# Kernel tuning notes

Hardware: AMD Instinct MI355X
Metric: run time of the kernel (lower is better)

## Reference

```python
import jax, jax.numpy as jnp
import numpy as np
from jax import lax

C = 768
SHIFT_DISTANCES = (1, 2, 3)


def _layernorm(x, g, b, eps=1e-5):
    m = jnp.mean(x, axis=-1, keepdims=True)
    v = jnp.mean((x - m) ** 2, axis=-1, keepdims=True)
    return (x - m) * lax.rsqrt(v + eps) * g + b


def setup_inputs() -> dict:
    key = jax.random.key(0)
    ks = jax.random.split(key, 16)
    B, T, N = 8, 16, 197
    inp = {
        "x": jax.random.normal(ks[0], (B * T, N, C), dtype=jnp.float32),
        "ln_g": jnp.ones((C,), jnp.float32),
        "ln_b": jnp.zeros((C,), jnp.float32),
        "gate_w": jax.random.normal(ks[1], (C, C), jnp.float32) * 0.02,
        "gate_b": jnp.zeros((C,), jnp.float32),
        "proj_w1": jax.random.normal(ks[2], (C, C), jnp.float32) * 0.02,
        "proj_b1": jnp.zeros((C,), jnp.float32),
        "proj_w2": jax.random.normal(ks[3], (C, C), jnp.float32) * 0.02,
        "proj_b2": jnp.zeros((C,), jnp.float32),
        "fusion_w": jnp.ones((len(SHIFT_DISTANCES),), jnp.float32),
        "num_frames": T,
    }
    for i, d in enumerate(SHIFT_DISTANCES):
        k = 2 * d + 1
        # depthwise Conv1d weight: (out=C, in/groups=1, k)
        inp[f"conv_w{i}"] = jax.random.normal(ks[4 + i], (C, 1, k), jnp.float32) * (1.0 / np.sqrt(k))
        inp[f"conv_b{i}"] = jnp.zeros((C,), jnp.float32)
    return inp


def _branch(x4, conv_w, conv_b, d, ln_g, ln_b, gate_w, gate_b):
    # x4: [B, T, N, C]
    B, T, N, Cc = x4.shape
    p = Cc // 3  # past / future split; static gets the remainder
    x_norm = jax.nn.relu(_layernorm(x4, ln_g, ln_b))
    # [B, T, N, C] -> [B*N, C, T] for depthwise conv over time
    x_1d = x_norm.transpose(0, 2, 3, 1).reshape(B * N, Cc, T)
    feat = lax.conv_general_dilated(
        x_1d, conv_w, window_strides=(1,), padding=[(d, d)],
        dimension_numbers=("NCH", "OIH", "NCH"), feature_group_count=Cc,
    ) + conv_b[None, :, None]
    feat = feat.reshape(B, N, Cc, T).transpose(0, 3, 1, 2)  # [B, T, N, C]
    gate = jax.nn.sigmoid(jnp.einsum("btnc,cd->btnd", feat, gate_w) + gate_b)
    y = gate * x4  # channelwise split-and-multiply fuses into one op
    y_past, y_future, y_static = y[..., :p], y[..., p:2 * p], y[..., 2 * p:]
    s = min(d, T)
    out_past = jnp.pad(y_past[:, s:], ((0, 0), (0, s), (0, 0), (0, 0)))  # lshift
    out_future = jnp.pad(y_future[:, :T - s], ((0, 0), (s, 0), (0, 0), (0, 0)))  # rshift
    return jnp.concatenate([out_past, out_future, y_static], axis=-1)


def reference(x, ln_g, ln_b, gate_w, gate_b, proj_w1, proj_b1, proj_w2, proj_b2,
              fusion_w, conv_w0, conv_b0, conv_w1, conv_b1, conv_w2, conv_b2,
              num_frames):
    B_T, N, Cc = x.shape
    T = num_frames
    B = B_T // T
    x4 = x.reshape(B, T, N, Cc)
    convs = [(conv_w0, conv_b0), (conv_w1, conv_b1), (conv_w2, conv_b2)]
    outs = jnp.stack([
        _branch(x4, cw, cb, d, ln_g, ln_b, gate_w, gate_b)
        for (cw, cb), d in zip(convs, SHIFT_DISTANCES)
    ], axis=0)  # [3, B, T, N, C]
    w = jax.nn.softmax(fusion_w)[:, None, None, None, None]
    fused = jnp.sum(w * outs, axis=0).reshape(B_T, N, Cc)
    h = jnp.einsum("bnc,cd->bnd", fused, proj_w1) + proj_b1
    h = jax.nn.gelu(h, approximate=False)
    h = jnp.einsum("bnc,cd->bnd", h, proj_w2) + proj_b2
    return x + h
```

## Files before the change

### kernel.cpp

```cpp
#include <hip/hip_runtime.h>
#include <math.h>


#define MROWS 25216
#define CD    768
#define NTOK  197
#define TFR   16

typedef __attribute__((ext_vector_type(8))) short short8;
typedef __attribute__((ext_vector_type(4))) float floatx4;
typedef unsigned int u32;

__device__ __forceinline__ unsigned short f2bf(float f) {
    union { float f; unsigned u; } v; v.f = f;
    unsigned r = v.u + 0x7FFFu + ((v.u >> 16) & 1u);
    return (unsigned short)(r >> 16);
}
__device__ __forceinline__ float bf2f(unsigned short h) {
    union { unsigned u; float f; } v; v.u = ((unsigned)h) << 16;
    return v.f;
}

__device__ __forceinline__ void gl2lds16(const void* g, void* l) {
    __builtin_amdgcn_global_load_lds(
        (__attribute__((address_space(1))) void*)(unsigned long long)g,
        (__attribute__((address_space(3))) void*)(u32)(unsigned long long)l,
        16, 0, 0);
}

__global__ __launch_bounds__(256)
void ln_relu_kernel(const float* __restrict__ x, const float* __restrict__ g,
                    const float* __restrict__ b, unsigned short* __restrict__ xn,
                    unsigned short* __restrict__ xb) {
    int row = blockIdx.x;
    int tid = threadIdx.x;
    const float* xr = x + (size_t)row * CD;
    float v0 = xr[tid], v1 = xr[tid + 256], v2 = xr[tid + 512];
    float s = v0 + v1 + v2;
    __shared__ float red[8];
#pragma unroll
    for (int off = 32; off; off >>= 1) s += __shfl_down(s, off, 64);
    int lane = tid & 63, w = tid >> 6;
    if (lane == 0) red[w] = s;
    __syncthreads();
    float mean = (red[0] + red[1] + red[2] + red[3]) * (1.0f / CD);
    float d0 = v0 - mean, d1 = v1 - mean, d2 = v2 - mean;
    float s2 = d0 * d0 + d1 * d1 + d2 * d2;
#pragma unroll
    for (int off = 32; off; off >>= 1) s2 += __shfl_down(s2, off, 64);
    if (lane == 0) red[4 + w] = s2;
    __syncthreads();
    float var = (red[4] + red[5] + red[6] + red[7]) * (1.0f / CD);
    float inv = rsqrtf(var + 1e-5f);
    unsigned short* xo = xn + (size_t)row * CD;
    unsigned short* xc = xb + (size_t)row * CD;
    float o0 = fmaxf(d0 * inv * g[tid]       + b[tid],       0.0f);
    float o1 = fmaxf(d1 * inv * g[tid + 256] + b[tid + 256], 0.0f);
    float o2 = fmaxf(d2 * inv * g[tid + 512] + b[tid + 512], 0.0f);
    xo[tid] = f2bf(o0); xo[tid + 256] = f2bf(o1); xo[tid + 512] = f2bf(o2);
    xc[tid] = f2bf(v0); xc[tid + 256] = f2bf(v1); xc[tid + 512] = f2bf(v2);
}

template <int D>
__device__ __forceinline__
void dw_body(const unsigned short* __restrict__ xn, const float* __restrict__ cw,
             const float* __restrict__ cb, unsigned short* __restrict__ feat) {
    constexpr int KK = 2 * D + 1;
    int gid = blockIdx.x * 256 + threadIdx.x;
    int bn = gid / 96;
    int cg = gid - bn * 96;
    int c0 = cg * 8;
    int b = bn / NTOK;
    size_t base = ((size_t)b * TFR * NTOK + (bn - b * NTOK)) * CD + c0;
    const size_t tstride = (size_t)NTOK * CD;

    short8 u[TFR];
#pragma unroll
    for (int t = 0; t < TFR; ++t)
        u[t] = *(const short8*)(xn + base + (size_t)t * tstride);

    float wgt[8][KK], bb[8];
#pragma unroll
    for (int q = 0; q < 8; ++q) {
        bb[q] = cb[c0 + q];
#pragma unroll
        for (int j = 0; j < KK; ++j) wgt[q][j] = cw[(c0 + q) * KK + j];
    }

#pragma unroll
    for (int t = 0; t < TFR; ++t) {
        float acc[8];
#pragma unroll
        for (int q = 0; q < 8; ++q) acc[q] = bb[q];
#pragma unroll
        for (int j = 0; j < KK; ++j) {
            int tj = t + j - D;
            if (tj < 0 || tj >= TFR) continue;
#pragma unroll
            for (int q = 0; q < 8; ++q)
                acc[q] += bf2f((unsigned short)u[tj][q]) * wgt[q][j];
        }
        short8 o;
#pragma unroll
        for (int q = 0; q < 8; ++q) o[q] = (short)f2bf(acc[q]);
        *(short8*)(feat + base + (size_t)t * tstride) = o;
    }
}

__global__ __launch_bounds__(256)
void dwconv_all(const unsigned short* __restrict__ xn,
                const float* __restrict__ cw0, const float* __restrict__ cb0,
                const float* __restrict__ cw1, const float* __restrict__ cb1,
                const float* __restrict__ cw2, const float* __restrict__ cb2,
                unsigned short* __restrict__ f1, unsigned short* __restrict__ f2,
                unsigned short* __restrict__ f3) {
    if (blockIdx.y == 0)      dw_body<1>(xn, cw0, cb0, f1);
    else if (blockIdx.y == 1) dw_body<2>(xn, cw1, cb1, f2);
    else                      dw_body<3>(xn, cw2, cb2, f3);
}

__global__ __launch_bounds__(256)
void wprep3_kernel(const float* __restrict__ w0, const float* __restrict__ w1,
                   const float* __restrict__ w2, unsigned short* __restrict__ t0,
                   unsigned short* __restrict__ t1, unsigned short* __restrict__ t2) {
    const float* w = blockIdx.y == 0 ? w0 : blockIdx.y == 1 ? w1 : w2;
    unsigned short* wt = blockIdx.y == 0 ? t0 : blockIdx.y == 1 ? t1 : t2;
    int gid = blockIdx.x * 256 + threadIdx.x;
    int n = gid / CD, k = gid - n * CD;
    wt[gid] = f2bf(w[(size_t)k * CD + n]);
}

__global__ __launch_bounds__(256)
void fuse_kernel(const unsigned short* __restrict__ y1,
                 const unsigned short* __restrict__ y2,
                 const unsigned short* __restrict__ y3,
                 unsigned short* __restrict__ fused) {
    int gid = blockIdx.x * 256 + threadIdx.x;
    int m = gid / 96;
    int kk = (gid - m * 96) * 8;
    int t = (m / NTOK) & 15;
    float vals[8] = {0.f, 0.f, 0.f, 0.f, 0.f, 0.f, 0.f, 0.f};
    const unsigned short* ys[3] = {y1, y2, y3};
#pragma unroll
    for (int d = 1; d <= 3; ++d) {
        int src; bool ok;
        if (kk < 256)      { src = m + d * NTOK; ok = (t + d) < TFR; }
        else if (kk < 512) { src = m - d * NTOK; ok = (t - d) >= 0; }
        else               { src = m;            ok = true; }
        if (ok) {
            short8 u = *(const short8*)(ys[d - 1] + (size_t)src * CD + kk);
#pragma unroll
            for (int e = 0; e < 8; ++e) vals[e] += bf2f((unsigned short)u[e]);
        }
    }
    short8 o;
#pragma unroll
    for (int e = 0; e < 8; ++e) o[e] = (short)f2bf(vals[e]);
    *(short8*)(fused + (size_t)m * CD + kk) = o;
}

template <int EPI>
__global__ __launch_bounds__(256)
void gemm_kernel(const unsigned short* __restrict__ A,
                 const unsigned short* __restrict__ Bt,
                 const float* __restrict__ bias,
                 const unsigned short* __restrict__ xb,
                 const float* __restrict__ xf,
                 float* __restrict__ outf,
                 unsigned short* __restrict__ outh0,
                 unsigned short* __restrict__ outh1,
                 unsigned short* __restrict__ outh2,
                 const float* __restrict__ fw) {
    __shared__ __align__(16) char smem[65536];
    unsigned short (*As)[128 * 32] = (unsigned short (*)[128 * 32])smem;
    unsigned short (*Bs)[128 * 32] = (unsigned short (*)[128 * 32])(smem + 32768);
    float (*fE)[132] = (float (*)[132])smem;

    int tid  = threadIdx.x;
    int m0   = blockIdx.x * 128;
    int n0   = blockIdx.y * 128;
    int widx = blockIdx.x / (MROWS / 128);
    int wave = tid >> 6, lane = tid & 63;
    int wm   = (wave >> 1) * 64, wn = (wave & 1) * 64;
    int quad = lane >> 4, l16 = lane & 15;
    int r4   = lane >> 2;
    int ckx  = (((lane & 3) ^ ((lane >> 3) & 3)) * 8);
    int rdsl = (quad ^ ((l16 >> 1) & 3)) * 8;

    const size_t arow = (size_t)(m0 + wave * 16 + r4) * CD + ckx;
    const size_t brow = (size_t)(n0 + wave * 16 + r4) * CD + ckx;
    const size_t skip = (size_t)64 * CD;

    floatx4 acc[4][4];
#pragma unroll
    for (int i = 0; i < 4; ++i)
#pragma unroll
        for (int j = 0; j < 4; ++j) acc[i][j] = (floatx4){0.f, 0.f, 0.f, 0.f};

    auto stage_h = [&](int t, int b, int h) {
        const size_t ko = (size_t)t * 32;
        gl2lds16(A  + arow + h * skip + ko, &As[b][(wave + h * 4) * 512]);
        gl2lds16(Bt + brow + h * skip + ko, &Bs[b][(wave + h * 4) * 512]);
    };
    auto stage = [&](int t, int b) { stage_h(t, b, 0); stage_h(t, b, 1); };

    constexpr int NT = CD / 32;

    auto kstep = [&](int t, bool doStage) {
        int b = t & 3;
        short8 af[4], bfr[4];
#pragma unroll
        for (int i = 0; i < 4; ++i)
            af[i] = *(const short8*)(&As[b][(wm + i * 16 + l16) * 32 + rdsl]);
        bfr[0] = *(const short8*)(&Bs[b][(wn + 0 * 16 + l16) * 32 + rdsl]);
        bfr[1] = *(const short8*)(&Bs[b][(wn + 1 * 16 + l16) * 32 + rdsl]);
        if (doStage) stage_h(t + 3, (t + 3) & 3, 0);
        asm volatile("s_waitcnt lgkmcnt(0)" ::: "memory");
        __builtin_amdgcn_sched_barrier(0);
        __builtin_amdgcn_s_setprio(1);
#pragma unroll
        for (int i = 0; i < 4; ++i) {
            acc[i][0] = __builtin_amdgcn_mfma_f32_16x16x32_bf16(af[i], bfr[0], acc[i][0], 0, 0, 0);
            acc[i][1] = __builtin_amdgcn_mfma_f32_16x16x32_bf16(af[i], bfr[1], acc[i][1], 0, 0, 0);
        }
        __builtin_amdgcn_s_setprio(0);
        __builtin_amdgcn_s_barrier();
        __builtin_amdgcn_sched_barrier(0);
        bfr[2] = *(const short8*)(&Bs[b][(wn + 2 * 16 + l16) * 32 + rdsl]);
        bfr[3] = *(const short8*)(&Bs[b][(wn + 3 * 16 + l16) * 32 + rdsl]);
        if (doStage) stage_h(t + 3, (t + 3) & 3, 1);
        asm volatile("s_waitcnt lgkmcnt(0)" ::: "memory");
        __builtin_amdgcn_sched_barrier(0);
        __builtin_amdgcn_s_setprio(1);
#pragma unroll
        for (int i = 0; i < 4; ++i) {
            acc[i][2] = __builtin_amdgcn_mfma_f32_16x16x32_bf16(af[i], bfr[2], acc[i][2], 0, 0, 0);
            acc[i][3] = __builtin_amdgcn_mfma_f32_16x16x32_bf16(af[i], bfr[3], acc[i][3], 0, 0, 0);
        }
        __builtin_amdgcn_s_setprio(0);
    };

    stage(0, 0);
    stage(1, 1);
    stage(2, 2);
    for (int t = 0; t < NT - 2; ++t) {
        asm volatile("s_waitcnt vmcnt(8)" ::: "memory");
        __builtin_amdgcn_s_barrier();
        __builtin_amdgcn_sched_barrier(0);
        kstep(t, t + 3 < NT);
    }
    asm volatile("s_waitcnt vmcnt(4)" ::: "memory");
    __builtin_amdgcn_s_barrier();
    __builtin_amdgcn_sched_barrier(0);
    kstep(NT - 2, false);
    asm volatile("s_waitcnt vmcnt(0)" ::: "memory");
    __builtin_amdgcn_s_barrier();
    __builtin_amdgcn_sched_barrier(0);
    kstep(NT - 1, false);

    float wd = 0.f;
    unsigned short* outh = outh0;
    if (EPI == 0) {
        float f0 = fw[0], f1 = fw[1], f2 = fw[2];
        float mx = fmaxf(f0, fmaxf(f1, f2));
        float e0 = expf(f0 - mx), e1 = expf(f1 - mx), e2 = expf(f2 - mx);
        float inv = 1.f / (e0 + e1 + e2);
        wd = (widx == 0 ? e0 : widx == 1 ? e1 : e2) * inv;
        outh = widx == 0 ? outh0 : widx == 1 ? outh1 : outh2;
    }
    const size_t lshift = (size_t)widx * MROWS * CD;

#pragma unroll
    for (int p = 0; p < 2; ++p) {
        __syncthreads();
        if (wm == p * 64) {
#pragma unroll
            for (int j = 0; j < 4; ++j) {
                int col = wn + j * 16 + l16;
                float bc = bias[n0 + col];
#pragma unroll
                for (int i = 0; i < 4; ++i)
#pragma unroll
                    for (int r = 0; r < 4; ++r)
                        fE[i * 16 + quad * 4 + r][col] = acc[i][j][r] + bc;
            }
        }
        __syncthreads();
#pragma unroll
        for (int it = 0; it < 4; ++it) {
            int lr   = it * 16 + (tid >> 4);
            int cg   = tid & 15;
            size_t grow = (size_t)(m0 + p * 64 + lr);
            int gcol = n0 + cg * 8;
            size_t idx = grow * CD + gcol - lshift;
            floatx4 v0 = *(const floatx4*)&fE[lr][cg * 8];
            floatx4 v1 = *(const floatx4*)&fE[lr][cg * 8 + 4];
            if (EPI == 0) {
                short8 xv = *(const short8*)(xb + idx);
                short8 o;
#pragma unroll
                for (int e = 0; e < 8; ++e) {
                    float vv = e < 4 ? v0[e] : v1[e - 4];
                    float gte = 1.f / (1.f + expf(-vv));
                    o[e] = (short)f2bf(wd * gte * bf2f((unsigned short)xv[e]));
                }
                *(short8*)(outh + idx) = o;
            } else if (EPI == 1) {
                short8 o;
#pragma unroll
                for (int e = 0; e < 8; ++e) {
                    float vv = e < 4 ? v0[e] : v1[e - 4];
                    float gl = 0.5f * vv * (1.0f + erff(vv * 0.70710678118f));
                    o[e] = (short)f2bf(gl);
                }
                *(short8*)(outh + idx) = o;
            } else {
                floatx4 x0 = *(const floatx4*)(xf + idx);
                floatx4 x1 = *(const floatx4*)(xf + idx + 4);
#pragma unroll
                for (int e = 0; e < 4; ++e) { v0[e] += x0[e]; v1[e] += x1[e]; }
                *(floatx4*)(outf + idx)     = v0;
                *(floatx4*)(outf + idx + 4) = v1;
            }
        }
    }
}

extern "C" void kernel_launch(void* const* d_in, const int* in_sizes, int n_in,
                              void* d_out, int out_size, void* d_ws, size_t ws_size,
                              hipStream_t stream) {
    const float* x      = (const float*)d_in[0];
    const float* ln_g   = (const float*)d_in[1];
    const float* ln_b   = (const float*)d_in[2];
    const float* gate_w = (const float*)d_in[3];
    const float* gate_b = (const float*)d_in[4];
    const float* pw1    = (const float*)d_in[5];
    const float* pb1    = (const float*)d_in[6];
    const float* pw2    = (const float*)d_in[7];
    const float* pb2    = (const float*)d_in[8];
    const float* fw     = (const float*)d_in[9];
    const float* cw[3]  = {(const float*)d_in[11], (const float*)d_in[13], (const float*)d_in[15]};
    const float* cb[3]  = {(const float*)d_in[12], (const float*)d_in[14], (const float*)d_in[16]};

    char* ws = (char*)d_ws;
    const size_t SB = (size_t)MROWS * CD * 2;
    unsigned short* gwt  = (unsigned short*)(ws + 0);
    unsigned short* p1t  = (unsigned short*)(ws + 1179648);
    unsigned short* p2t  = (unsigned short*)(ws + 2359296);
    unsigned short* xn   = (unsigned short*)(ws + 3538944);
    unsigned short* xb   = (unsigned short*)(ws + 3538944 + SB);
    unsigned short* f1   = (unsigned short*)(ws + 3538944 + 2 * SB);
    unsigned short* f2   = (unsigned short*)(ws + 3538944 + 3 * SB);
    unsigned short* f3   = (unsigned short*)(ws + 3538944 + 4 * SB);
    unsigned short* y1    = xn;
    unsigned short* y2    = f1;
    unsigned short* y3    = f2;
    unsigned short* fused = f3;
    unsigned short* h1    = xn;

    dim3 wg(2304, 3);
    wprep3_kernel<<<wg, 256, 0, stream>>>(gate_w, pw1, pw2, gwt, p1t, p2t);
    ln_relu_kernel<<<MROWS, 256, 0, stream>>>(x, ln_g, ln_b, xn, xb);

    dim3 dg(591, 3);
    dwconv_all<<<dg, 256, 0, stream>>>(xn, cw[0], cb[0], cw[1], cb[1], cw[2], cb[2],
                                       f1, f2, f3);

    dim3 gg3(591, 6);
    unsigned short* y2s = (unsigned short*)(ws + 3538944 + 5 * SB);
    unsigned short* y3s = (unsigned short*)(ws + 3538944 + 6 * SB);
    gemm_kernel<0><<<gg3, 256, 0, stream>>>(f1, gwt, gate_b, xb, nullptr,
                                            nullptr, y1, y2s, y3s, fw);

    fuse_kernel<<<9456, 256, 0, stream>>>(y1, y2s, y3s, fused);

    dim3 gg(197, 6);
    gemm_kernel<1><<<gg, 256, 0, stream>>>(fused, p1t, pb1, nullptr, nullptr,
                                           nullptr, h1, nullptr, nullptr, nullptr);
    gemm_kernel<2><<<gg, 256, 0, stream>>>(h1, p2t, pb2, nullptr, x,
                                           (float*)d_out, nullptr, nullptr, nullptr, nullptr);
}
```

Measured before the change: 549.5 us.

## Enlarge GEMM tiles to 128x256 with 8 waves, BK=64 and triple buffering

Rewrites the bf16 MFMA GEMM to use 128x256 output tiles computed by 512 threads (8 waves in a 2x4 layout), a K step of 64 with a new XOR swizzle, and a 3-stage LDS ring in 144 KB of dynamic shared memory. The goal is more reuse of each A tile across output columns and fewer, larger K iterations, which cuts global traffic and barriers per FLOP. The cost is one block per CU because of the large LDS footprint, a grid half as wide along N, and a wider single-pass epilogue staging area.

```diff
diff --git a/kernel.cpp b/kernel.cpp
--- a/kernel.cpp
+++ b/kernel.cpp
@@ -160,7 +160,7 @@
 }
 
 template <int EPI>
-__global__ __launch_bounds__(256)
+__global__ __launch_bounds__(512)
 void gemm_kernel(const unsigned short* __restrict__ A,
                  const unsigned short* __restrict__ Bt,
                  const float* __restrict__ bias,
@@ -171,25 +171,15 @@
                  unsigned short* __restrict__ outh1,
                  unsigned short* __restrict__ outh2,
                  const float* __restrict__ fw) {
-    __shared__ __align__(16) char smem[65536];
-    unsigned short (*As)[128 * 32] = (unsigned short (*)[128 * 32])smem;
-    unsigned short (*Bs)[128 * 32] = (unsigned short (*)[128 * 32])(smem + 32768);
-    float (*fE)[132] = (float (*)[132])smem;
-
+    extern __shared__ __align__(16) char smem[];
     int tid  = threadIdx.x;
     int m0   = blockIdx.x * 128;
-    int n0   = blockIdx.y * 128;
-    int widx = blockIdx.x / (MROWS / 128);
+    int n0   = blockIdx.y * 256;
     int wave = tid >> 6, lane = tid & 63;
-    int wm   = (wave >> 1) * 64, wn = (wave & 1) * 64;
+    int wr   = wave >> 2, wc = wave & 3;
     int quad = lane >> 4, l16 = lane & 15;
-    int r4   = lane >> 2;
-    int ckx  = (((lane & 3) ^ ((lane >> 3) & 3)) * 8);
-    int rdsl = (quad ^ ((l16 >> 1) & 3)) * 8;
-
-    const size_t arow = (size_t)(m0 + wave * 16 + r4) * CD + ckx;
-    const size_t brow = (size_t)(n0 + wave * 16 + r4) * CD + ckx;
-    const size_t skip = (size_t)64 * CD;
+    int rr   = lane >> 3;
+    int ckx  = ((lane & 7) ^ rr) * 8;
 
     floatx4 acc[4][4];
 #pragma unroll
@@ -197,68 +187,98 @@
 #pragma unroll
         for (int j = 0; j < 4; ++j) acc[i][j] = (floatx4){0.f, 0.f, 0.f, 0.f};
 
-    auto stage_h = [&](int t, int b, int h) {
-        const size_t ko = (size_t)t * 32;
-        gl2lds16(A  + arow + h * skip + ko, &As[b][(wave + h * 4) * 512]);
-        gl2lds16(Bt + brow + h * skip + ko, &Bs[b][(wave + h * 4) * 512]);
+    auto Asb = [&](int bb) { return (unsigned short*)(smem + bb * 16384); };
+    auto Bsb = [&](int bb) { return (unsigned short*)(smem + 49152 + bb * 32768); };
+
+    auto sA = [&](int t, int bb, int h) {
+        int q = wave + h * 8;
+        gl2lds16(A + (size_t)(m0 + q * 8 + rr) * CD + t * 64 + ckx, Asb(bb) + q * 512);
     };
-    auto stage = [&](int t, int b) { stage_h(t, b, 0); stage_h(t, b, 1); };
-
-    constexpr int NT = CD / 32;
+    auto sB = [&](int t, int bb, int h) {
+        int q = wave + h * 8;
+        gl2lds16(Bt + (size_t)(n0 + q * 8 + rr) * CD + t * 64 + ckx, Bsb(bb) + q * 512);
+    };
+    auto ldA = [&](int bb, int i, int kk) -> short8 {
+        int r = wr * 64 + i * 16 + l16;
+        int slot = (kk * 4 + quad) ^ (l16 & 7);
+        return *(const short8*)((const char*)Asb(bb) + r * 128 + slot * 16);
+    };
+    auto ldB = [&](int bb, int j, int kk) -> short8 {
+        int r = wc * 64 + j * 16 + l16;
+        int slot = (kk * 4 + quad) ^ (l16 & 7);
+        return *(const short8*)((const char*)Bsb(bb) + r * 128 + slot * 16);
+    };
+
+#define LGKM0 do { asm volatile("s_waitcnt lgkmcnt(0)" ::: "memory"); \
+                   __builtin_amdgcn_sched_barrier(0); } while (0)
+#define PBAR  do { __builtin_amdgcn_s_barrier(); \
+                   __builtin_amdgcn_sched_barrier(0); } while (0)
 
     auto kstep = [&](int t, bool doStage) {
-        int b = t & 3;
-        short8 af[4], bfr[4];
-#pragma unroll
-        for (int i = 0; i < 4; ++i)
-            af[i] = *(const short8*)(&As[b][(wm + i * 16 + l16) * 32 + rdsl]);
-        bfr[0] = *(const short8*)(&Bs[b][(wn + 0 * 16 + l16) * 32 + rdsl]);
-        bfr[1] = *(const short8*)(&Bs[b][(wn + 1 * 16 + l16) * 32 + rdsl]);
-        if (doStage) stage_h(t + 3, (t + 3) & 3, 0);
-        asm volatile("s_waitcnt lgkmcnt(0)" ::: "memory");
-        __builtin_amdgcn_sched_barrier(0);
+        int bb = t % 3, bn = (t + 2) % 3;
+        short8 a0[4], a1[4], u, v;
+#pragma unroll
+        for (int i = 0; i < 4; ++i) a0[i] = ldA(bb, i, 0);
+        u = ldB(bb, 0, 0); v = ldB(bb, 1, 0);
+        if (doStage) { sA(t + 2, bn, 0); sA(t + 2, bn, 1); }
+        LGKM0;
         __builtin_amdgcn_s_setprio(1);
 #pragma unroll
         for (int i = 0; i < 4; ++i) {
-            acc[i][0] = __builtin_amdgcn_mfma_f32_16x16x32_bf16(af[i], bfr[0], acc[i][0], 0, 0, 0);
-            acc[i][1] = __builtin_amdgcn_mfma_f32_16x16x32_bf16(af[i], bfr[1], acc[i][1], 0, 0, 0);
+            acc[i][0] = __builtin_amdgcn_mfma_f32_16x16x32_bf16(a0[i], u, acc[i][0], 0, 0, 0);
+            acc[i][1] = __builtin_amdgcn_mfma_f32_16x16x32_bf16(a0[i], v, acc[i][1], 0, 0, 0);
         }
         __builtin_amdgcn_s_setprio(0);
-        __builtin_amdgcn_s_barrier();
-        __builtin_amdgcn_sched_barrier(0);
-        bfr[2] = *(const short8*)(&Bs[b][(wn + 2 * 16 + l16) * 32 + rdsl]);
-        bfr[3] = *(const short8*)(&Bs[b][(wn + 3 * 16 + l16) * 32 + rdsl]);
-        if (doStage) stage_h(t + 3, (t + 3) & 3, 1);
-        asm volatile("s_waitcnt lgkmcnt(0)" ::: "memory");
-        __builtin_amdgcn_sched_barrier(0);
+        PBAR;
+        u = ldB(bb, 2, 0); v = ldB(bb, 3, 0);
+        if (doStage) { sB(t + 2, bn, 0); sB(t + 2, bn, 1); }
+        LGKM0;
         __builtin_amdgcn_s_setprio(1);
 #pragma unroll
         for (int i = 0; i < 4; ++i) {
-            acc[i][2] = __builtin_amdgcn_mfma_f32_16x16x32_bf16(af[i], bfr[2], acc[i][2], 0, 0, 0);
-            acc[i][3] = __builtin_amdgcn_mfma_f32_16x16x32_bf16(af[i], bfr[3], acc[i][3], 0, 0, 0);
+            acc[i][2] = __builtin_amdgcn_mfma_f32_16x16x32_bf16(a0[i], u, acc[i][2], 0, 0, 0);
+            acc[i][3] = __builtin_amdgcn_mfma_f32_16x16x32_bf16(a0[i], v, acc[i][3], 0, 0, 0);
+        }
+        __builtin_amdgcn_s_setprio(0);
+        PBAR;
+#pragma unroll
+        for (int i = 0; i < 4; ++i) a1[i] = ldA(bb, i, 1);
+        u = ldB(bb, 0, 1); v = ldB(bb, 1, 1);
+        if (doStage) { sB(t + 2, bn, 2); sB(t + 2, bn, 3); }
+        LGKM0;
+        __builtin_amdgcn_s_setprio(1);
+#pragma unroll
+        for (int i = 0; i < 4; ++i) {
+            acc[i][0] = __builtin_amdgcn_mfma_f32_16x16x32_bf16(a1[i], u, acc[i][0], 0, 0, 0);
+            acc[i][1] = __builtin_amdgcn_mfma_f32_16x16x32_bf16(a1[i], v, acc[i][1], 0, 0, 0);
+        }
+        __builtin_amdgcn_s_setprio(0);
+        PBAR;
+        u = ldB(bb, 2, 1); v = ldB(bb, 3, 1);
+        LGKM0;
+        __builtin_amdgcn_s_setprio(1);
+#pragma unroll
+        for (int i = 0; i < 4; ++i) {
+            acc[i][2] = __builtin_amdgcn_mfma_f32_16x16x32_bf16(a1[i], u, acc[i][2], 0, 0, 0);
+            acc[i][3] = __builtin_amdgcn_mfma_f32_16x16x32_bf16(a1[i], v, acc[i][3], 0, 0, 0);
         }
         __builtin_amdgcn_s_setprio(0);
     };
 
-    stage(0, 0);
-    stage(1, 1);
-    stage(2, 2);
-    for (int t = 0; t < NT - 2; ++t) {
-        asm volatile("s_waitcnt vmcnt(8)" ::: "memory");
-        __builtin_amdgcn_s_barrier();
-        __builtin_amdgcn_sched_barrier(0);
-        kstep(t, t + 3 < NT);
-    }
-    asm volatile("s_waitcnt vmcnt(4)" ::: "memory");
-    __builtin_amdgcn_s_barrier();
-    __builtin_amdgcn_sched_barrier(0);
-    kstep(NT - 2, false);
+    constexpr int NT = CD / 64;
+    sA(0, 0, 0); sA(0, 0, 1); sB(0, 0, 0); sB(0, 0, 1); sB(0, 0, 2); sB(0, 0, 3);
+    sA(1, 1, 0); sA(1, 1, 1); sB(1, 1, 0); sB(1, 1, 1); sB(1, 1, 2); sB(1, 1, 3);
+    for (int t = 0; t < NT - 1; ++t) {
+        asm volatile("s_waitcnt vmcnt(6)" ::: "memory");
+        PBAR;
+        kstep(t, t + 2 < NT);
+    }
     asm volatile("s_waitcnt vmcnt(0)" ::: "memory");
-    __builtin_amdgcn_s_barrier();
-    __builtin_amdgcn_sched_barrier(0);
+    PBAR;
     kstep(NT - 1, false);
 
     float wd = 0.f;
+    int widx = (EPI == 0) ? (blockIdx.x / 197) : 0;
     unsigned short* outh = outh0;
     if (EPI == 0) {
         float f0 = fw[0], f1 = fw[1], f2 = fw[2];
@@ -268,62 +288,59 @@
         wd = (widx == 0 ? e0 : widx == 1 ? e1 : e2) * inv;
         outh = widx == 0 ? outh0 : widx == 1 ? outh1 : outh2;
     }
-    const size_t lshift = (size_t)widx * MROWS * CD;
-
-#pragma unroll
-    for (int p = 0; p < 2; ++p) {
-        __syncthreads();
-        if (wm == p * 64) {
-#pragma unroll
-            for (int j = 0; j < 4; ++j) {
-                int col = wn + j * 16 + l16;
-                float bc = bias[n0 + col];
-#pragma unroll
-                for (int i = 0; i < 4; ++i)
-#pragma unroll
-                    for (int r = 0; r < 4; ++r)
-                        fE[i * 16 + quad * 4 + r][col] = acc[i][j][r] + bc;
+
+    float (*fE)[268] = (float (*)[268])smem;
+    __syncthreads();
+#pragma unroll
+    for (int j = 0; j < 4; ++j) {
+        int col = wc * 64 + j * 16 + l16;
+        float bc = bias[n0 + col];
+#pragma unroll
+        for (int i = 0; i < 4; ++i)
+#pragma unroll
+            for (int r = 0; r < 4; ++r)
+                fE[wr * 64 + i * 16 + quad * 4 + r][col] = acc[i][j][r] + bc;
+    }
+    __syncthreads();
+#pragma unroll
+    for (int it = 0; it < 8; ++it) {
+        int lr = it * 16 + (tid >> 5);
+        int cg = tid & 31;
+        size_t lrow = (size_t)(m0 + lr) - (size_t)widx * MROWS;
+        int gcol = n0 + cg * 8;
+        size_t idx = lrow * CD + gcol;
+        floatx4 v0 = *(const floatx4*)&fE[lr][cg * 8];
+        floatx4 v1 = *(const floatx4*)&fE[lr][cg * 8 + 4];
+        if (EPI == 0) {
+            short8 xv = *(const short8*)(xb + idx);
+            short8 o;
+#pragma unroll
+            for (int e = 0; e < 8; ++e) {
+                float vv = e < 4 ? v0[e] : v1[e - 4];
+                float gte = 1.f / (1.f + expf(-vv));
+                o[e] = (short)f2bf(wd * gte * bf2f((unsigned short)xv[e]));
             }
-        }
-        __syncthreads();
-#pragma unroll
-        for (int it = 0; it < 4; ++it) {
-            int lr   = it * 16 + (tid >> 4);
-            int cg   = tid & 15;
-            size_t grow = (size_t)(m0 + p * 64 + lr);
-            int gcol = n0 + cg * 8;
-            size_t idx = grow * CD + gcol - lshift;
-            floatx4 v0 = *(const floatx4*)&fE[lr][cg * 8];
-            floatx4 v1 = *(const floatx4*)&fE[lr][cg * 8 + 4];
-            if (EPI == 0) {
-                short8 xv = *(const short8*)(xb + idx);
-                short8 o;
-#pragma unroll
-                for (int e = 0; e < 8; ++e) {
-                    float vv = e < 4 ? v0[e] : v1[e - 4];
-                    float gte = 1.f / (1.f + expf(-vv));
-                    o[e] = (short)f2bf(wd * gte * bf2f((unsigned short)xv[e]));
-                }
-                *(short8*)(outh + idx) = o;
-            } else if (EPI == 1) {
-                short8 o;
-#pragma unroll
-                for (int e = 0; e < 8; ++e) {
-                    float vv = e < 4 ? v0[e] : v1[e - 4];
-                    float gl = 0.5f * vv * (1.0f + erff(vv * 0.70710678118f));
-                    o[e] = (short)f2bf(gl);
-                }
-                *(short8*)(outh + idx) = o;
-            } else {
-                floatx4 x0 = *(const floatx4*)(xf + idx);
-                floatx4 x1 = *(const floatx4*)(xf + idx + 4);
-#pragma unroll
-                for (int e = 0; e < 4; ++e) { v0[e] += x0[e]; v1[e] += x1[e]; }
-                *(floatx4*)(outf + idx)     = v0;
-                *(floatx4*)(outf + idx + 4) = v1;
+            *(short8*)(outh + idx) = o;
+        } else if (EPI == 1) {
+            short8 o;
+#pragma unroll
+            for (int e = 0; e < 8; ++e) {
+                float vv = e < 4 ? v0[e] : v1[e - 4];
+                float gl = 0.5f * vv * (1.0f + erff(vv * 0.70710678118f));
+                o[e] = (short)f2bf(gl);
             }
-        }
-    }
+            *(short8*)(outh + idx) = o;
+        } else {
+            floatx4 x0 = *(const floatx4*)(xf + idx);
+            floatx4 x1 = *(const floatx4*)(xf + idx + 4);
+#pragma unroll
+            for (int e = 0; e < 4; ++e) { v0[e] += x0[e]; v1[e] += x1[e]; }
+            *(floatx4*)(outf + idx)     = v0;
+            *(floatx4*)(outf + idx + 4) = v1;
+        }
+    }
+#undef LGKM0
+#undef PBAR
 }
 
 extern "C" void kernel_launch(void* const* d_in, const int* in_sizes, int n_in,
@@ -352,11 +369,19 @@
     unsigned short* f1   = (unsigned short*)(ws + 3538944 + 2 * SB);
     unsigned short* f2   = (unsigned short*)(ws + 3538944 + 3 * SB);
     unsigned short* f3   = (unsigned short*)(ws + 3538944 + 4 * SB);
+    unsigned short* y2s  = (unsigned short*)(ws + 3538944 + 5 * SB);
+    unsigned short* y3s  = (unsigned short*)(ws + 3538944 + 6 * SB);
     unsigned short* y1    = xn;
-    unsigned short* y2    = f1;
-    unsigned short* y3    = f2;
     unsigned short* fused = f3;
     unsigned short* h1    = xn;
+
+    const int LDSB = 147456;
+    hipFuncSetAttribute(reinterpret_cast<const void*>(gemm_kernel<0>),
+                        hipFuncAttributeMaxDynamicSharedMemorySize, LDSB);
+    hipFuncSetAttribute(reinterpret_cast<const void*>(gemm_kernel<1>),
+                        hipFuncAttributeMaxDynamicSharedMemorySize, LDSB);
+    hipFuncSetAttribute(reinterpret_cast<const void*>(gemm_kernel<2>),
+                        hipFuncAttributeMaxDynamicSharedMemorySize, LDSB);
 
     dim3 wg(2304, 3);
     wprep3_kernel<<<wg, 256, 0, stream>>>(gate_w, pw1, pw2, gwt, p1t, p2t);
@@ -366,17 +391,15 @@
     dwconv_all<<<dg, 256, 0, stream>>>(xn, cw[0], cb[0], cw[1], cb[1], cw[2], cb[2],
                                        f1, f2, f3);
 
-    dim3 gg3(591, 6);
-    unsigned short* y2s = (unsigned short*)(ws + 3538944 + 5 * SB);
-    unsigned short* y3s = (unsigned short*)(ws + 3538944 + 6 * SB);
-    gemm_kernel<0><<<gg3, 256, 0, stream>>>(f1, gwt, gate_b, xb, nullptr,
-                                            nullptr, y1, y2s, y3s, fw);
+    dim3 gg3(591, 3);
+    gemm_kernel<0><<<gg3, 512, LDSB, stream>>>(f1, gwt, gate_b, xb, nullptr,
+                                               nullptr, y1, y2s, y3s, fw);
 
     fuse_kernel<<<9456, 256, 0, stream>>>(y1, y2s, y3s, fused);
 
-    dim3 gg(197, 6);
-    gemm_kernel<1><<<gg, 256, 0, stream>>>(fused, p1t, pb1, nullptr, nullptr,
-                                           nullptr, h1, nullptr, nullptr, nullptr);
-    gemm_kernel<2><<<gg, 256, 0, stream>>>(h1, p2t, pb2, nullptr, x,
-                                           (float*)d_out, nullptr, nullptr, nullptr, nullptr);
-}
+    dim3 gg(197, 3);
+    gemm_kernel<1><<<gg, 512, LDSB, stream>>>(fused, p1t, pb1, nullptr, nullptr,
+                                              nullptr, h1, nullptr, nullptr, nullptr);
+    gemm_kernel<2><<<gg, 512, LDSB, stream>>>(h1, p2t, pb2, nullptr, x,
+                                              (float*)d_out, nullptr, nullptr, nullptr, nullptr);
+}
```

After: 529.2 us. -3.7%, faster.
